# Performance work log

Measured on AMD Instinct MI355X. Metric: run time of the kernel, lower is better.

## Reference

```python
import jax, jax.numpy as jnp
import numpy as np
import math

B_, S_, D_ = 8, 2048, 512
N_ = 16
EXPAND = 1.5
INNER = math.ceil(D_ * EXPAND)  # 768
K_ = 3
DELTA_MIN = 1e-4
DELTA_MAX = 3.0


def _hippo(n):
    A = np.zeros((n, n), np.float32)
    for i in range(n):
        ci = math.sqrt(2 * i + 1)
        for m in range(i + 1):
            cm = math.sqrt(2 * m + 1)
            if i == m:
                A[i, m] = -(2 * i + 1)
            else:
                A[i, m] = (-1.0 if (i - m) % 2 == 0 else 1.0) * ci * cm
    idx = np.arange(n, dtype=np.float32)
    Bv = np.sqrt(2.0 * idx + 1.0)
    Cv = Bv.copy()
    Cv[1::2] *= -1.0
    return A, Bv, Cv


def setup_inputs() -> dict:
    key = jax.random.key(0)
    k0, k1, k2, k3 = jax.random.split(key, 4)
    A0, Bv, Cv = _hippo(N_)
    scale = 1.0 / math.sqrt(INNER)
    return {
        "x": jax.random.normal(k0, (B_, S_, D_), jnp.float32),
        "ln_g": jnp.ones((D_,), jnp.float32),
        "ln_b": jnp.zeros((D_,), jnp.float32),
        "W_in": jax.random.normal(k1, (3 * INNER, D_), jnp.float32) / math.sqrt(D_),
        "conv_w": jax.random.normal(k2, (INNER, 1, K_), jnp.float32) / math.sqrt(K_),
        "A": jnp.asarray(A0),
        "Bmat": jnp.asarray(np.repeat(Bv[:, None], INNER, axis=1) * scale),  # (N, inner)
        "Cmat": jnp.asarray(np.repeat(Cv[None, :], INNER, axis=0) * scale),  # (inner, N)
        "W_out": jax.random.normal(k3, (D_, INNER), jnp.float32) / math.sqrt(INNER),
    }


def reference(x, ln_g, ln_b, W_in, conv_w, A, Bmat, Cmat, W_out):
    B, S, D = x.shape
    N = A.shape[0]
    # LayerNorm
    mu = jnp.mean(x, -1, keepdims=True)
    var = jnp.var(x, -1, keepdims=True)
    h = (x - mu) / jnp.sqrt(var + 1e-5) * ln_g + ln_b
    # Input projection -> data / gate / delta_raw
    proj = h @ W_in.T  # (B,S,3*inner)
    inner = proj.shape[-1] // 3
    data, gate, delta_raw = jnp.split(proj, 3, axis=-1)
    # Depthwise conv with padding K-1 then truncation to S == causal left pad K-1
    K = conv_w.shape[-1]
    dc = jax.lax.conv_general_dilated(
        data.transpose(0, 2, 1), conv_w, window_strides=(1,),
        padding=[(K - 1, 0)], dimension_numbers=("NCH", "OIH", "NCH"),
        feature_group_count=inner,
    ).transpose(0, 2, 1)  # (B,S,inner)
    u = jax.nn.silu(dc)
    # Data-dependent step size
    delta = jnp.mean(jax.nn.softplus(delta_raw), -1, keepdims=True) + DELTA_MIN
    delta = jnp.minimum(delta, DELTA_MAX)  # (B,S,1)
    # ZOH discretisation: A_disc = expm(delta*A); B_disc = A^{-1}(A_disc - I) B
    scaled_A = delta[..., None] * A  # (B,S,N,N)
    A_disc = jax.vmap(jax.scipy.linalg.expm)(scaled_A.reshape(-1, N, N)).reshape(B, S, N, N)
    rhs = A_disc - jnp.eye(N, dtype=x.dtype)
    integral = jnp.linalg.solve(jnp.broadcast_to(A, rhs.shape), rhs)  # (B,S,N,N)
    B_disc = integral @ Bmat  # (B,S,N,inner)

    def step(state, inputs):  # state: (B,N)
        Ad, Bd, ut = inputs  # (B,N,N), (B,N,inner), (B,inner)
        state = jnp.einsum("bnm,bm->bn", Ad, state) + jnp.einsum("bnd,bd->bn", Bd, ut)
        y = jnp.einsum("dn,bn->bd", Cmat, state)  # (B,inner)
        return state, y

    s0 = jnp.zeros((B, N), x.dtype)
    _, ys = jax.lax.scan(
        step, s0,
        (A_disc.transpose(1, 0, 2, 3), B_disc.transpose(1, 0, 2, 3), u.transpose(1, 0, 2)),
    )
    selective = ys.transpose(1, 0, 2)  # (B,S,inner)
    out = (jax.nn.sigmoid(gate) * selective) @ W_out.T
    return x + out
```

## Files before the change

### kernel.cpp

```cpp
#include <hip/hip_runtime.h>
#include <hip/hip_bf16.h>
#include <math.h>

#define BB 8
#define SS 2048
#define DD 512
#define II 768
#define MT (BB*SS)
#define NS 16
#define CH 32
#define NCB (SS/CH)
#define NCHK (MT/CH)
#define NT 1024

typedef __hip_bfloat16 bf16;
typedef __attribute__((ext_vector_type(8))) short bf16x8;
typedef __attribute__((ext_vector_type(4))) float f32x4;

__device__ __forceinline__ float fsigm(float x){
  return __builtin_amdgcn_rcpf(1.f + __expf(-x));
}
__device__ __forceinline__ float fsoftp(float x){
  return (x > 15.f) ? x : __logf(1.f + __expf(x));
}
__device__ __forceinline__ unsigned short f2bf_bits(float f){
  __hip_bfloat16 h = __float2bfloat16(f);
  return __builtin_bit_cast(unsigned short, h);
}
__device__ __forceinline__ float bfbits2f(short s){
  union { float f; unsigned u; } v;
  v.u = ((unsigned)(unsigned short)s) << 16;
  return v.f;
}
__device__ __forceinline__ void gload16(const bf16* src, void* dst){
  __builtin_amdgcn_global_load_lds((const __attribute__((address_space(1))) void*)src,
                                   (__attribute__((address_space(3))) void*)dst, 16, 0, 0);
}
__device__ __forceinline__ void gload16f(const float* src, void* dst){
  __builtin_amdgcn_global_load_lds((const __attribute__((address_space(1))) void*)src,
                                   (__attribute__((address_space(3))) void*)dst, 16, 0, 0);
}
template<int KDIM>
__device__ __forceinline__ bf16x8 lds_a_frag(const bf16* As, int row, int kseg){
  return *(const bf16x8*)((const char*)As + (size_t)row*(KDIM*2)
                          + (size_t)((kseg ^ (row & 7)) << 4));
}

__global__ __launch_bounds__(256) void cast_kernel(
    const float* __restrict__ in, bf16* __restrict__ out, int n4)
{
  int i = blockIdx.x*256 + threadIdx.x;
  if (i >= n4) return;
  float4 v = *(const float4*)&in[(size_t)i*4];
  ushort4 o = make_ushort4(f2bf_bits(v.x), f2bf_bits(v.y), f2bf_bits(v.z), f2bf_bits(v.w));
  *(ushort4*)&out[(size_t)i*4] = o;
}

__global__ __launch_bounds__(256) void bmsplit_kernel(
    const float* __restrict__ Bm, bf16* __restrict__ hi, bf16* __restrict__ lo)
{
  int i = blockIdx.x*256 + threadIdx.x;
  if (i >= NS*II) return;
  float f = Bm[i];
  unsigned short hb = f2bf_bits(f);
  hi[i] = __builtin_bit_cast(bf16, hb);
  lo[i] = __float2bfloat16(f - bfbits2f((short)hb));
}

__global__ __launch_bounds__(256) void apow_kernel(
    const float* __restrict__ A, float* __restrict__ Apow)
{
  __shared__ double Am[256], T0[256], T1[256];
  __shared__ double colsum[16];
  int tid = threadIdx.x, r = tid>>4, c = tid&15;
  double a = (double)A[tid];
  Am[tid] = a; T0[tid] = a;
  Apow[tid] = A[tid];
  __syncthreads();
  double *Tc = T0, *Tn = T1;
  for (int k=2;k<=13;k++){
    double s = 0.0;
    #pragma unroll
    for (int j=0;j<16;j++) s += Tc[r*16+j]*Am[j*16+c];
    Tn[tid] = s;
    Apow[(k-1)*256 + tid] = (float)s;
    __syncthreads();
    double* tmp = Tc; Tc = Tn; Tn = tmp;
  }
  if (tid < 16){
    double s = 0.0;
    #pragma unroll
    for (int j=0;j<16;j++) s += fabs(Am[j*16+tid]);
    colsum[tid] = s;
  }
  __syncthreads();
  if (tid == 0){
    double mx = 0.0;
    #pragma unroll
    for (int j=0;j<16;j++) mx = fmax(mx, colsum[j]);
    Apow[13*256] = (float)mx;
  }
}

__global__ __launch_bounds__(64) void etab_kernel(
    const float* __restrict__ Apow, float* __restrict__ Etab,
    float* __restrict__ Gtab, float* __restrict__ dEtab)
{
  int i = blockIdx.x;
  int l = threadIdx.x;
  int r = l&15, gq = l>>4, c0 = gq*4;
  __shared__ alignas(16) float bufE[256];
  __shared__ alignas(16) float bufG[256];
  float delta = (3.0f*i)/(float)(NT-1);
  float anorm = Apow[13*256];
  float mx = delta*anorm;
  int s = 0;
  if (mx > 2.f){
    s = (int)ceilf(log2f(mx)) - 1;
    if (s < 0) s = 0;
    if (s > 12) s = 12;
  }
  float dsc = ldexpf(delta, -s);
  const float invk[14]  = {0.f, 1.f, 0.5f, 1.f/3.f, 0.25f, 0.2f, 1.f/6.f, 1.f/7.f,
                           0.125f, 1.f/9.f, 0.1f, 1.f/11.f, 1.f/12.f, 1.f/13.f};
  float4 e = make_float4(0.f,0.f,0.f,0.f), g = e;
  if (r==c0  ){ e.x = 1.f; g.x = dsc; }
  if (r==c0+1){ e.y = 1.f; g.y = dsc; }
  if (r==c0+2){ e.z = 1.f; g.z = dsc; }
  if (r==c0+3){ e.w = 1.f; g.w = dsc; }
  float ck = 1.f;
  #pragma unroll
  for (int k=1;k<=13;k++){
    ck *= dsc * invk[k];
    float gk = ck * dsc / (float)(k+1);
    float4 ap = *(const float4*)&Apow[(k-1)*256 + r*16 + c0];
    e.x = fmaf(ck, ap.x, e.x); e.y = fmaf(ck, ap.y, e.y);
    e.z = fmaf(ck, ap.z, e.z); e.w = fmaf(ck, ap.w, e.w);
    g.x = fmaf(gk, ap.x, g.x); g.y = fmaf(gk, ap.y, g.y);
    g.z = fmaf(gk, ap.z, g.z); g.w = fmaf(gk, ap.w, g.w);
  }
  for (int it=0; it<s; ++it){
    *(float4*)&bufE[r*16+c0] = e;
    *(float4*)&bufG[r*16+c0] = g;
    __syncthreads();
    float erow[16];
    #pragma unroll
    for (int q4=0;q4<4;q4++){
      float4 tv = *(const float4*)&bufE[r*16+q4*4];
      erow[q4*4+0]=tv.x; erow[q4*4+1]=tv.y; erow[q4*4+2]=tv.z; erow[q4*4+3]=tv.w;
    }
    float4 en = make_float4(0.f,0.f,0.f,0.f);
    float4 gn = g;
    #pragma unroll
    for (int kk=0;kk<16;kk++){
      float4 ev = *(const float4*)&bufE[kk*16+c0];
      float4 gv = *(const float4*)&bufG[kk*16+c0];
      float ek = erow[kk];
      en.x=fmaf(ek,ev.x,en.x); en.y=fmaf(ek,ev.y,en.y);
      en.z=fmaf(ek,ev.z,en.z); en.w=fmaf(ek,ev.w,en.w);
      gn.x=fmaf(ek,gv.x,gn.x); gn.y=fmaf(ek,gv.y,gn.y);
      gn.z=fmaf(ek,gv.z,gn.z); gn.w=fmaf(ek,gv.w,gn.w);
    }
    e = en; g = gn;
    __syncthreads();
  }
  size_t o = (size_t)i*256 + r*16 + c0;
  *(float4*)&Etab[o] = e;
  *(float4*)&Gtab[o] = g;
  *(float4*)&bufE[r*16+c0] = e;
  __syncthreads();
  float4 de = make_float4(0.f,0.f,0.f,0.f);
  #pragma unroll
  for (int q4=0;q4<4;q4++){
    float4 ar = *(const float4*)&Apow[r*16 + q4*4];
    float4 e0 = *(const float4*)&bufE[(q4*4+0)*16 + c0];
    float4 e1 = *(const float4*)&bufE[(q4*4+1)*16 + c0];
    float4 e2 = *(const float4*)&bufE[(q4*4+2)*16 + c0];
    float4 e3 = *(const float4*)&bufE[(q4*4+3)*16 + c0];
    de.x = fmaf(ar.x,e0.x,fmaf(ar.y,e1.x,fmaf(ar.z,e2.x,fmaf(ar.w,e3.x,de.x))));
    de.y = fmaf(ar.x,e0.y,fmaf(ar.y,e1.y,fmaf(ar.z,e2.y,fmaf(ar.w,e3.y,de.y))));
    de.z = fmaf(ar.x,e0.z,fmaf(ar.y,e1.z,fmaf(ar.z,e2.z,fmaf(ar.w,e3.z,de.z))));
    de.w = fmaf(ar.x,e0.w,fmaf(ar.y,e1.w,fmaf(ar.z,e2.w,fmaf(ar.w,e3.w,de.w))));
  }
  *(float4*)&dEtab[o] = de;
}

__global__ __launch_bounds__(256) void ln_kernel(
    const float* __restrict__ x, const float* __restrict__ g,
    const float* __restrict__ b, bf16* __restrict__ h)
{
  int w = threadIdx.x >> 6, l = threadIdx.x & 63;
  int m = blockIdx.x*4 + w;
  const float* xr = x + (size_t)m*DD;
  float4 v0 = *(const float4*)&xr[l*4];
  float4 v1 = *(const float4*)&xr[256 + l*4];
  float s  = v0.x+v0.y+v0.z+v0.w + v1.x+v1.y+v1.z+v1.w;
  float sq = v0.x*v0.x+v0.y*v0.y+v0.z*v0.z+v0.w*v0.w
           + v1.x*v1.x+v1.y*v1.y+v1.z*v1.z+v1.w*v1.w;
  #pragma unroll
  for (int o=1;o<64;o<<=1){ s += __shfl_xor(s,o); sq += __shfl_xor(sq,o); }
  float mu  = s*(1.f/DD);
  float var = sq*(1.f/DD) - mu*mu;
  float rs  = rsqrtf(var + 1e-5f);
  float4 g0 = *(const float4*)&g[l*4];
  float4 b0 = *(const float4*)&b[l*4];
  float4 g1 = *(const float4*)&g[256 + l*4];
  float4 b1 = *(const float4*)&b[256 + l*4];
  ushort4 o0, o1;
  o0.x = f2bf_bits((v0.x-mu)*rs*g0.x + b0.x);
  o0.y = f2bf_bits((v0.y-mu)*rs*g0.y + b0.y);
  o0.z = f2bf_bits((v0.z-mu)*rs*g0.z + b0.z);
  o0.w = f2bf_bits((v0.w-mu)*rs*g0.w + b0.w);
  o1.x = f2bf_bits((v1.x-mu)*rs*g1.x + b1.x);
  o1.y = f2bf_bits((v1.y-mu)*rs*g1.y + b1.y);
  o1.z = f2bf_bits((v1.z-mu)*rs*g1.z + b1.z);
  o1.w = f2bf_bits((v1.w-mu)*rs*g1.w + b1.w);
  *(ushort4*)&h[(size_t)m*DD + l*4]       = o0;
  *(ushort4*)&h[(size_t)m*DD + 256 + l*4] = o1;
}


__global__ __launch_bounds__(256, 3) void gemm1_mfma(
    const bf16* __restrict__ Ah, const bf16* __restrict__ Bw,
    bf16* __restrict__ databf, bf16* __restrict__ gatebf, float* __restrict__ dacc)
{
  __shared__ alignas(16) bf16 As[128*64];
  __shared__ alignas(16) bf16 Bs[128*64];
  const int tid = threadIdx.x, l = tid & 63, w = tid >> 6;
  const int lrow = l & 15, lgrp = l >> 4;
  const int orig = blockIdx.x;
  const int swz = (orig & 7) * (2304/8) + (orig >> 3);
  const int bm = (swz / 18) * 128;
  const int bn = swz % 18;
  const int wrow = (w >> 1) * 64, wcol = (w & 1) * 64;

  f32x4 acc[4][4];
  #pragma unroll
  for (int i=0;i<4;i++){
    #pragma unroll
    for (int f=0;f<4;f++){ f32x4 z={0.f,0.f,0.f,0.f}; acc[i][f]=z; }
  }

  for (int t=0; t<8; ++t){
    #pragma unroll
    for (int it=0; it<4; ++it){
      int d = tid + it*256;
      int r = d >> 3, s = d & 7;
      gload16(Ah + (size_t)(bm + r)*DD + t*64 + ((s ^ (r&7))<<3),
              (char*)As + (size_t)(d - l)*16);
    }
    #pragma unroll
    for (int it=0; it<4; ++it){
      int d = tid + it*256;
      int r = d >> 3, s = d & 7;
      gload16(Bw + (size_t)(bn*128 + r)*DD + t*64 + ((s ^ (r&7))<<3),
              (char*)Bs + (size_t)(d - l)*16);
    }
    __syncthreads();
    #pragma unroll
    for (int kk=0; kk<2; ++kk){
      bf16x8 afr[4], bfr[4];
      #pragma unroll
      for (int i=0;i<4;i++) afr[i] = lds_a_frag<64>(As, wrow + i*16 + lrow, kk*4 + lgrp);
      #pragma unroll
      for (int f=0;f<4;f++) bfr[f] = lds_a_frag<64>(Bs, wcol + f*16 + lrow, kk*4 + lgrp);
      #pragma unroll
      for (int i=0;i<4;i++){
        #pragma unroll
        for (int f=0;f<4;f++)
          acc[i][f] = __builtin_amdgcn_mfma_f32_16x16x32_bf16(afr[i], bfr[f], acc[i][f], 0,0,0);
      }
    }
    __syncthreads();
  }

  const int rowb = bm + wrow + lgrp*4;
  const int cglob = bn*128 + wcol + lrow;
  if (bn < 6){
    #pragma unroll
    for (int i=0;i<4;i++){
      #pragma unroll
      for (int f=0;f<4;f++){
        int col = cglob + f*16;
        #pragma unroll
        for (int j=0;j<4;j++)
          databf[(size_t)(rowb + i*16 + j)*II + col] = __float2bfloat16(acc[i][f][j]);
      }
    }
  } else if (bn < 12){
    #pragma unroll
    for (int i=0;i<4;i++){
      #pragma unroll
      for (int f=0;f<4;f++){
        int col = cglob - 768 + f*16;
        #pragma unroll
        for (int j=0;j<4;j++)
          gatebf[(size_t)(rowb + i*16 + j)*II + col] = __float2bfloat16(fsigm(acc[i][f][j]));
      }
    }
  } else {
    #pragma unroll
    for (int i=0;i<4;i++){
      #pragma unroll
      for (int j=0;j<4;j++){
        float v = fsoftp(acc[i][0][j]) + fsoftp(acc[i][1][j])
                + fsoftp(acc[i][2][j]) + fsoftp(acc[i][3][j]);
        v += __shfl_xor(v,1); v += __shfl_xor(v,2);
        v += __shfl_xor(v,4); v += __shfl_xor(v,8);
        if (lrow == 0) atomicAdd(&dacc[rowb + i*16 + j], v);
      }
    }
  }
}

__global__ __launch_bounds__(256, 3) void gemm2_mfma(
    const bf16* __restrict__ Asel, const bf16* __restrict__ Bw,
    const float* __restrict__ x, float* __restrict__ out)
{
  __shared__ alignas(16) bf16 As[128*64];
  __shared__ alignas(16) bf16 Bs[128*64];
  const int tid = threadIdx.x, l = tid & 63, w = tid >> 6;
  const int lrow = l & 15, lgrp = l >> 4;
  const int orig = blockIdx.x;
  const int swz = (orig & 7) * (512/8) + (orig >> 3);
  const int bm = (swz >> 2) * 128;
  const int bn = swz & 3;
  const int wrow = (w >> 1) * 64, wcol = (w & 1) * 64;

  f32x4 acc[4][4];
  #pragma unroll
  for (int i=0;i<4;i++){
    #pragma unroll
    for (int f=0;f<4;f++){ f32x4 z={0.f,0.f,0.f,0.f}; acc[i][f]=z; }
  }

  for (int t=0; t<12; ++t){
    #pragma unroll
    for (int it=0; it<4; ++it){
      int d = tid + it*256;
      int r = d >> 3, s = d & 7;
      gload16(Asel + (size_t)(bm + r)*II + t*64 + ((s ^ (r&7))<<3),
              (char*)As + (size_t)(d - l)*16);
    }
    #pragma unroll
    for (int it=0; it<4; ++it){
      int d = tid + it*256;
      int r = d >> 3, s = d & 7;
      gload16(Bw + (size_t)(bn*128 + r)*II + t*64 + ((s ^ (r&7))<<3),
              (char*)Bs + (size_t)(d - l)*16);
    }
    __syncthreads();
    #pragma unroll
    for (int kk=0; kk<2; ++kk){
      bf16x8 afr[4], bfr[4];
      #pragma unroll
      for (int i=0;i<4;i++) afr[i] = lds_a_frag<64>(As, wrow + i*16 + lrow, kk*4 + lgrp);
      #pragma unroll
      for (int f=0;f<4;f++) bfr[f] = lds_a_frag<64>(Bs, wcol + f*16 + lrow, kk*4 + lgrp);
      #pragma unroll
      for (int i=0;i<4;i++){
        #pragma unroll
        for (int f=0;f<4;f++)
          acc[i][f] = __builtin_amdgcn_mfma_f32_16x16x32_bf16(afr[i], bfr[f], acc[i][f], 0,0,0);
      }
    }
    __syncthreads();
  }

  const int rowb = bm + wrow + lgrp*4;
  #pragma unroll
  for (int i=0;i<4;i++){
    #pragma unroll
    for (int f=0;f<4;f++){
      int col = bn*128 + wcol + f*16 + lrow;
      #pragma unroll
      for (int j=0;j<4;j++){
        size_t e = (size_t)(rowb + i*16 + j)*DD + col;
        out[e] = acc[i][f][j] + x[e];
      }
    }
  }
}

__global__ __launch_bounds__(256) void convw_mfma(
    const bf16* __restrict__ data, const float* __restrict__ cw,
    const bf16* __restrict__ Bmhi, const bf16* __restrict__ Bmlo,
    float* __restrict__ w_all)
{
  __shared__ alignas(16) bf16  Ds[1728*8];
  __shared__ alignas(16) float cwl[II*3];
  __shared__ alignas(16) float red[4][256];
  const int tid = threadIdx.x, l = tid & 63, wv = tid >> 6;
  const int lrow = l & 15, lgrp = l >> 4;
  const int p0 = blockIdx.x * 16;
  const int p  = p0 + lrow;
  const int t  = p & (SS-1);
  const int bstart = p0 & ~(SS-1);
  const float mask1 = (t>=1) ? 1.f : 0.f;
  const float mask0 = (t>=2) ? 1.f : 0.f;

  #pragma unroll
  for (int it=0; it<7; ++it){
    int d = tid + it*256;
    if (d < 1728){
      int r = d % 18, s2 = d / 18;
      int prow = p0 - 2 + r; if (prow < bstart) prow = bstart;
      gload16(data + (size_t)prow*II + s2*8, (char*)Ds + (size_t)(d - l)*16);
    }
  }
  #pragma unroll
  for (int it=0; it<3; ++it){
    int d = tid + it*256;
    if (d < 576)
      gload16f(cw + d*4, (char*)cwl + (size_t)(d - l)*16);
  }
  __syncthreads();

  const int sB = wv*24 + lgrp;
  const char* DsB = (const char*)Ds + ((size_t)sB*18 + lrow)*16;
  const bf16* bh  = Bmhi + (size_t)lrow*II + sB*8;
  const bf16* bl  = Bmlo + (size_t)lrow*II + sB*8;
  const float* cwp = cwl + sB*24;

  f32x4 acc = {0.f,0.f,0.f,0.f};
  #pragma unroll
  for (int u=0; u<6; ++u){
    bf16x8 v0 = *(const bf16x8*)(DsB + (size_t)u*72*16);
    bf16x8 v1 = *(const bf16x8*)(DsB + (size_t)u*72*16 + 16);
    bf16x8 v2 = *(const bf16x8*)(DsB + (size_t)u*72*16 + 32);
    bf16x8 ah = *(const bf16x8*)(bh + u*32);
    bf16x8 al = *(const bf16x8*)(bl + u*32);
    float cv[24];
    #pragma unroll
    for (int q=0;q<6;q++){
      float4 cq = *(const float4*)(cwp + u*96 + q*4);
      cv[q*4+0]=cq.x; cv[q*4+1]=cq.y; cv[q*4+2]=cq.z; cv[q*4+3]=cq.w;
    }
    bf16x8 Bh, Bl;
    #pragma unroll
    for (int j=0;j<8;j++){
      float d2 = bfbits2f(v2[j]);
      float d1 = bfbits2f(v1[j]) * mask1;
      float d0 = bfbits2f(v0[j]) * mask0;
      float a = fmaf(d0, cv[3*j], fmaf(d1, cv[3*j+1], d2*cv[3*j+2]));
      float u2 = a * fsigm(a);
      unsigned short hb = f2bf_bits(u2);
      Bh[j] = (short)hb;
      Bl[j] = (short)f2bf_bits(u2 - bfbits2f((short)hb));
    }
    acc = __builtin_amdgcn_mfma_f32_16x16x32_bf16(ah, Bh, acc, 0,0,0);
    acc = __builtin_amdgcn_mfma_f32_16x16x32_bf16(ah, Bl, acc, 0,0,0);
    acc = __builtin_amdgcn_mfma_f32_16x16x32_bf16(al, Bh, acc, 0,0,0);
  }
  *(f32x4*)&red[wv][l*4] = acc;
  __syncthreads();
  if (wv == 0){
    f32x4 s0 = *(const f32x4*)&red[0][l*4];
    f32x4 s1 = *(const f32x4*)&red[1][l*4];
    f32x4 s2 = *(const f32x4*)&red[2][l*4];
    f32x4 s3 = *(const f32x4*)&red[3][l*4];
    f32x4 s = s0 + s1 + s2 + s3;
    *(f32x4*)&w_all[(size_t)p*NS + lgrp*4] = s;
  }
}

__global__ __launch_bounds__(256) void scan1_kernel(
    const float* __restrict__ Etab, const float* __restrict__ Gtab,
    const float* __restrict__ dEtab, const float* __restrict__ dacc,
    const float* __restrict__ w_all,
    float* __restrict__ Ad, float* __restrict__ c_all,
    float* __restrict__ P, float* __restrict__ q)
{
  int cc = blockIdx.x;
  int bb = cc / NCB, ci = cc % NCB;
  size_t base = (size_t)bb*SS + (size_t)ci*CH;
  int tid = threadIdx.x;
  int i = tid>>4, j = tid&15;
  __shared__ float Et[CH][256];
  __shared__ float cb[CH][16];
  __shared__ float Pb[2][256];
  __shared__ float qb[2][16];
  Pb[0][tid] = (i==j)?1.f:0.f;
  if (tid<16) qb[0][tid]=0.f;
  const float hh = 3.f/(float)(NT-1);
  for (int t=0;t<CH;t++){
    size_t m = base + t;
    float delta = fminf(dacc[m]*(1.f/II) + 1e-4f, 3.0f);
    float tf = delta * (float)(NT-1) * (1.f/3.f);
    int i0 = (int)tf;
    if (i0 > NT-2) i0 = NT-2;
    float fr = tf - (float)i0;
    float fr2 = fr*fr, fr3 = fr2*fr;
    float h00 = 2.f*fr3 - 3.f*fr2 + 1.f;
    float h10 = fr3 - 2.f*fr2 + fr;
    float h01 = -2.f*fr3 + 3.f*fr2;
    float h11 = fr3 - fr2;
    size_t o0 = (size_t)i0*256 + tid;
    float E0 = Etab[o0], E1 = Etab[o0+256];
    float D0 = dEtab[o0], D1 = dEtab[o0+256];
    float G0 = Gtab[o0], G1 = Gtab[o0+256];
    float e = h00*E0 + h01*E1 + hh*(h10*D0 + h11*D1);
    float g = h00*G0 + h01*G1 + hh*(h10*E0 + h11*E1);
    Ad[m*256 + tid] = e;
    Et[t][j*16 + i] = e;
    float cv = g * w_all[m*NS + j];
    cv += __shfl_xor(cv,1); cv += __shfl_xor(cv,2);
    cv += __shfl_xor(cv,4); cv += __shfl_xor(cv,8);
    if (j==0){ c_all[m*NS + i] = cv; cb[t][i] = cv; }
  }
  __syncthreads();
  int cur = 0;
  for (int t=0;t<CH;t++){
    float acc2 = 0.f;
    #pragma unroll
    for (int k=0;k<16;k++) acc2 = fmaf(Et[t][k*16+i], Pb[cur][k*16+j], acc2);
    float qa = 0.f;
    if (j==0){
      #pragma unroll
      for (int k=0;k<16;k++) qa = fmaf(Et[t][k*16+i], qb[cur][k], qa);
      qa += cb[t][i];
    }
    Pb[cur^1][tid] = acc2;
    if (j==0) qb[cur^1][i] = qa;
    __syncthreads();
    cur ^= 1;
  }
  P[(size_t)cc*256 + tid] = Pb[cur][tid];
  if (tid<16) q[(size_t)cc*NS + tid] = qb[cur][tid];
}

__global__ __launch_bounds__(64) void scan2_kernel(
    const float* __restrict__ P, const float* __restrict__ q,
    float* __restrict__ entry)
{
  int b = blockIdx.x;
  int l = threadIdx.x;
  __shared__ alignas(16) float Pl[2][256];
  __shared__ float el[2][16];
  if (l < 16) el[0][l] = 0.f;
  gload16f(P + (size_t)(b*NCB)*256 + l*4, (char*)Pl[0]);
  float qv = q[(size_t)(b*NCB)*NS + (l & 15)];
  int cur = 0;
  for (int ci=0; ci<NCB; ci++){
    __syncthreads();
    int cc = b*NCB + ci;
    if (ci+1 < NCB)
      gload16f(P + (size_t)(cc+1)*256 + l*4, (char*)Pl[cur^1]);
    float qn = (ci+1 < NCB) ? q[(size_t)(cc+1)*NS + (l&15)] : 0.f;
    if (l < 16){
      entry[(size_t)cc*NS + l] = el[cur][l];
      float a = qv;
      #pragma unroll
      for (int k=0;k<16;k++) a = fmaf(Pl[cur][l*16+k], el[cur][k], a);
      el[cur^1][l] = a;
    }
    qv = qn;
    cur ^= 1;
  }
}

__global__ __launch_bounds__(256) void scan3sel_kernel(
    const float* __restrict__ Ad, const float* __restrict__ c_all,
    const float* __restrict__ entry, const float* __restrict__ Cm,
    const bf16* __restrict__ gate, bf16* __restrict__ selg)
{
  __shared__ alignas(16) float Ads[CH*256];
  __shared__ alignas(16) float cl[CH*16];
  int cc = blockIdx.x;
  int bb = cc / NCB, ci = cc % NCB;
  size_t base = (size_t)bb*SS + (size_t)ci*CH;
  int tid = threadIdx.x, l = tid & 63, w = tid >> 6;
  int r = l & 15;
  const float* Adc = Ad + base*256;
  #pragma unroll
  for (int it=0; it<8; ++it){
    int d = tid + it*256;
    int tt = d >> 6, rr = (d >> 2) & 15, k4 = d & 3;
    gload16f(Adc + tt*256 + rr*16 + ((k4 ^ ((rr>>1)&3))<<2),
             (char*)Ads + (size_t)(d - l)*16);
  }
  {
    int d = tid;
    if (d < 128)
      gload16f(c_all + base*NS + d*4, (char*)cl + (size_t)(d - l)*16);
  }
  float g[16];
  #pragma unroll
  for (int k=0;k<16;k++) g[k] = entry[(size_t)cc*NS + k];
  __syncthreads();

  const int frm = (r>>1)&3;
  for (int t=0;t<CH;t++){
    size_t m = base + t;
    float s = cl[t*16 + r];
    #pragma unroll
    for (int q4=0;q4<4;q4++){
      float4 ev = *(const float4*)&Ads[(t*64 + r*4 + (q4 ^ frm))*4];
      s = fmaf(ev.x, g[q4*4+0], s);
      s = fmaf(ev.y, g[q4*4+1], s);
      s = fmaf(ev.z, g[q4*4+2], s);
      s = fmaf(ev.w, g[q4*4+3], s);
    }
    #pragma unroll
    for (int k=0;k<16;k++) g[k] = __shfl(s, k);
    #pragma unroll
    for (int p=0;p<3;p++){
      int jcol = w*192 + p*64 + l;
      float y = 0.f;
      #pragma unroll
      for (int q4=0;q4<4;q4++){
        float4 cv = *(const float4*)&Cm[jcol*16 + q4*4];
        y = fmaf(cv.x, g[q4*4+0], y);
        y = fmaf(cv.y, g[q4*4+1], y);
        y = fmaf(cv.z, g[q4*4+2], y);
        y = fmaf(cv.w, g[q4*4+3], y);
      }
      size_t e = m*II + jcol;
      float gv = __bfloat162float(gate[e]);
      selg[e] = __float2bfloat16(gv*y);
    }
  }
}

extern "C" void kernel_launch(void* const* d_in, const int* in_sizes, int n_in,
                              void* d_out, int out_size, void* d_ws, size_t ws_size,
                              hipStream_t stream) {
  (void)in_sizes; (void)n_in; (void)out_size; (void)ws_size;
  const float* x      = (const float*)d_in[0];
  const float* ln_g   = (const float*)d_in[1];
  const float* ln_b   = (const float*)d_in[2];
  const float* W_in   = (const float*)d_in[3];
  const float* conv_w = (const float*)d_in[4];
  const float* A      = (const float*)d_in[5];
  const float* Bm     = (const float*)d_in[6];
  const float* Cm     = (const float*)d_in[7];
  const float* Wout   = (const float*)d_in[8];
  float* out = (float*)d_out;

  char* ws = (char*)d_ws;
  size_t off = 0;
  #define WSALLOC(ty, name, count) \
    ty* name = (ty*)(ws + off); off += (((size_t)(count))*sizeof(ty) + 255) & ~(size_t)255;
  WSALLOC(bf16,  hbf,    (size_t)MT*DD)
  WSALLOC(bf16,  databf, (size_t)MT*II)
  WSALLOC(bf16,  gatebf, (size_t)MT*II)
  WSALLOC(float, dacc,   MT)
  WSALLOC(float, w_all,  (size_t)MT*NS)
  WSALLOC(float, Ad,     (size_t)MT*256)
  WSALLOC(float, c_all,  (size_t)MT*NS)
  WSALLOC(float, Pbuf,   (size_t)NCHK*256)
  WSALLOC(float, qbuf,   (size_t)NCHK*NS)
  WSALLOC(float, entry,  (size_t)NCHK*NS)
  WSALLOC(bf16,  Winbf,  (size_t)3*II*DD)
  WSALLOC(bf16,  Woutbf, (size_t)DD*II)
  WSALLOC(bf16,  Bmhi,   (size_t)NS*II)
  WSALLOC(bf16,  Bmlo,   (size_t)NS*II)
  WSALLOC(float, Apow,   13*256 + 16)
  WSALLOC(float, Etab,   (size_t)NT*256)
  WSALLOC(float, Gtab,   (size_t)NT*256)
  WSALLOC(float, dEtab,  (size_t)NT*256)
  #undef WSALLOC

  hipMemsetAsync(dacc, 0, (size_t)MT*sizeof(float), stream);
  cast_kernel  <<<(3*II*DD/4 + 255)/256, 256, 0, stream>>>(W_in,  Winbf,  3*II*DD/4);
  cast_kernel  <<<(DD*II/4   + 255)/256, 256, 0, stream>>>(Wout,  Woutbf, DD*II/4);
  bmsplit_kernel<<<(NS*II + 255)/256, 256, 0, stream>>>(Bm, Bmhi, Bmlo);
  apow_kernel  <<<1, 256, 0, stream>>>(A, Apow);
  etab_kernel  <<<NT, 64, 0, stream>>>(Apow, Etab, Gtab, dEtab);
  ln_kernel    <<<MT/4, 256, 0, stream>>>(x, ln_g, ln_b, hbf);
  gemm1_mfma   <<<dim3(2304), 256, 0, stream>>>(hbf, Winbf, databf, gatebf, dacc);
  convw_mfma   <<<MT/16, 256, 0, stream>>>(databf, conv_w, Bmhi, Bmlo, w_all);
  scan1_kernel <<<NCHK, 256, 0, stream>>>(Etab, Gtab, dEtab, dacc, w_all, Ad, c_all, Pbuf, qbuf);
  scan2_kernel <<<BB, 64, 0, stream>>>(Pbuf, qbuf, entry);
  scan3sel_kernel<<<NCHK, 256, 0, stream>>>(Ad, c_all, entry, Cm, gatebf, databf);
  gemm2_mfma   <<<dim3(512), 256, 0, stream>>>(databf, Woutbf, x, out);
}
```

Before: 206.9 us.

## Split scan3sel into single-wave state recurrence and parallel output phase

The chunk scan kernel now runs the 16-state recurrence in one wave only and stores each step's state into shared memory. After a barrier, all 256 threads compute the C-projection and gating for the 32 timesteps, each thread owning three contiguous columns whose C rows are held in registers. Before, every one of the four waves redundantly recomputed the recurrence and reloaded C from global memory at every step. The trade is a serial phase where three waves sit idle, plus strided per-thread gate and output accesses (three consecutive bf16 per thread) that may coalesce worse than the earlier lane-contiguous pattern.

```diff
diff --git a/kernel.cpp b/kernel.cpp
--- a/kernel.cpp
+++ b/kernel.cpp
@@ -566,10 +566,11 @@
 {
   __shared__ alignas(16) float Ads[CH*256];
   __shared__ alignas(16) float cl[CH*16];
+  __shared__ alignas(16) float Gs[CH][16];
   int cc = blockIdx.x;
   int bb = cc / NCB, ci = cc % NCB;
   size_t base = (size_t)bb*SS + (size_t)ci*CH;
-  int tid = threadIdx.x, l = tid & 63, w = tid >> 6;
+  int tid = threadIdx.x, l = tid & 63;
   int r = l & 15;
   const float* Adc = Ad + base*256;
   #pragma unroll
@@ -579,45 +580,61 @@
     gload16f(Adc + tt*256 + rr*16 + ((k4 ^ ((rr>>1)&3))<<2),
              (char*)Ads + (size_t)(d - l)*16);
   }
-  {
-    int d = tid;
-    if (d < 128)
-      gload16f(c_all + base*NS + d*4, (char*)cl + (size_t)(d - l)*16);
-  }
-  float g[16];
-  #pragma unroll
-  for (int k=0;k<16;k++) g[k] = entry[(size_t)cc*NS + k];
-  __syncthreads();
-
-  const int frm = (r>>1)&3;
+  if (tid < 128)
+    gload16f(c_all + base*NS + tid*4, (char*)cl + (size_t)(tid - l)*16);
+
+  float cmr[3][16];
+  #pragma unroll
+  for (int p=0;p<3;p++){
+    int jcol = tid*3 + p;
+    #pragma unroll
+    for (int q4=0;q4<4;q4++){
+      float4 cv = *(const float4*)&Cm[jcol*16 + q4*4];
+      cmr[p][q4*4+0]=cv.x; cmr[p][q4*4+1]=cv.y;
+      cmr[p][q4*4+2]=cv.z; cmr[p][q4*4+3]=cv.w;
+    }
+  }
+  __syncthreads();
+
+  if (tid < 64){
+    float g[16];
+    #pragma unroll
+    for (int k=0;k<16;k++) g[k] = entry[(size_t)cc*NS + k];
+    const int frm = (r>>1)&3;
+    for (int t=0;t<CH;t++){
+      float s = cl[t*16 + r];
+      #pragma unroll
+      for (int q4=0;q4<4;q4++){
+        float4 ev = *(const float4*)&Ads[(t*64 + r*4 + (q4 ^ frm))*4];
+        s = fmaf(ev.x, g[q4*4+0], s);
+        s = fmaf(ev.y, g[q4*4+1], s);
+        s = fmaf(ev.z, g[q4*4+2], s);
+        s = fmaf(ev.w, g[q4*4+3], s);
+      }
+      #pragma unroll
+      for (int k=0;k<16;k++) g[k] = __shfl(s, k);
+      if (l < 16) Gs[t][l] = s;
+    }
+  }
+  __syncthreads();
+
+  const int col0 = tid*3;
+  const bf16* gp = gate + base*II + col0;
+  bf16* sp = selg + base*II + col0;
   for (int t=0;t<CH;t++){
-    size_t m = base + t;
-    float s = cl[t*16 + r];
+    float gk[16];
     #pragma unroll
     for (int q4=0;q4<4;q4++){
-      float4 ev = *(const float4*)&Ads[(t*64 + r*4 + (q4 ^ frm))*4];
-      s = fmaf(ev.x, g[q4*4+0], s);
-      s = fmaf(ev.y, g[q4*4+1], s);
-      s = fmaf(ev.z, g[q4*4+2], s);
-      s = fmaf(ev.w, g[q4*4+3], s);
-    }
-    #pragma unroll
-    for (int k=0;k<16;k++) g[k] = __shfl(s, k);
+      float4 gv4 = *(const float4*)&Gs[t][q4*4];
+      gk[q4*4+0]=gv4.x; gk[q4*4+1]=gv4.y; gk[q4*4+2]=gv4.z; gk[q4*4+3]=gv4.w;
+    }
     #pragma unroll
     for (int p=0;p<3;p++){
-      int jcol = w*192 + p*64 + l;
       float y = 0.f;
       #pragma unroll
-      for (int q4=0;q4<4;q4++){
-        float4 cv = *(const float4*)&Cm[jcol*16 + q4*4];
-        y = fmaf(cv.x, g[q4*4+0], y);
-        y = fmaf(cv.y, g[q4*4+1], y);
-        y = fmaf(cv.z, g[q4*4+2], y);
-        y = fmaf(cv.w, g[q4*4+3], y);
-      }
-      size_t e = m*II + jcol;
-      float gv = __bfloat162float(gate[e]);
-      selg[e] = __float2bfloat16(gv*y);
+      for (int k=0;k<16;k++) y = fmaf(cmr[p][k], gk[k], y);
+      float gv = __bfloat162float(gp[(size_t)t*II + p]);
+      sp[(size_t)t*II + p] = __float2bfloat16(gv*y);
     }
   }
 }
```

Measured after the change: 211.8 us. 2.4% more time.

## Recompute discretised A in scan3 instead of storing it to global memory

Applied to the files above, without the earlier changes.

Drops the per-timestep 16x16 A_disc buffer that scan1 wrote to global memory and scan3 read back, and recomputes it in scan3 by interpolating the cached tables into a swizzled shared-memory layout. Also keeps each thread's Cmat rows in registers rather than reloading them every timestep. This removes a large global write and read, but duplicates the interpolation work and increases register pressure in scan3.

```diff
diff --git a/kernel.cpp b/kernel.cpp
--- a/kernel.cpp
+++ b/kernel.cpp
@@ -468,8 +468,7 @@
     const float* __restrict__ Etab, const float* __restrict__ Gtab,
     const float* __restrict__ dEtab, const float* __restrict__ dacc,
     const float* __restrict__ w_all,
-    float* __restrict__ Ad, float* __restrict__ c_all,
-    float* __restrict__ P, float* __restrict__ q)
+    float* __restrict__ c_all, float* __restrict__ P, float* __restrict__ q)
 {
   int cc = blockIdx.x;
   int bb = cc / NCB, ci = cc % NCB;
@@ -501,7 +500,6 @@
     float G0 = Gtab[o0], G1 = Gtab[o0+256];
     float e = h00*E0 + h01*E1 + hh*(h10*D0 + h11*D1);
     float g = h00*G0 + h01*G1 + hh*(h10*E0 + h11*E1);
-    Ad[m*256 + tid] = e;
     Et[t][j*16 + i] = e;
     float cv = g * w_all[m*NS + j];
     cv += __shfl_xor(cv,1); cv += __shfl_xor(cv,2);
@@ -560,7 +558,8 @@
 }
 
 __global__ __launch_bounds__(256) void scan3sel_kernel(
-    const float* __restrict__ Ad, const float* __restrict__ c_all,
+    const float* __restrict__ Etab, const float* __restrict__ dEtab,
+    const float* __restrict__ dacc, const float* __restrict__ c_all,
     const float* __restrict__ entry, const float* __restrict__ Cm,
     const bf16* __restrict__ gate, bf16* __restrict__ selg)
 {
@@ -571,18 +570,41 @@
   size_t base = (size_t)bb*SS + (size_t)ci*CH;
   int tid = threadIdx.x, l = tid & 63, w = tid >> 6;
   int r = l & 15;
-  const float* Adc = Ad + base*256;
-  #pragma unroll
-  for (int it=0; it<8; ++it){
-    int d = tid + it*256;
-    int tt = d >> 6, rr = (d >> 2) & 15, k4 = d & 3;
-    gload16f(Adc + tt*256 + rr*16 + ((k4 ^ ((rr>>1)&3))<<2),
-             (char*)Ads + (size_t)(d - l)*16);
-  }
-  {
-    int d = tid;
-    if (d < 128)
-      gload16f(c_all + base*NS + d*4, (char*)cl + (size_t)(d - l)*16);
+  int i = tid >> 4, j = tid & 15;
+  if (tid < 128)
+    gload16f(c_all + base*NS + tid*4, (char*)cl + (size_t)(tid - l)*16);
+
+  float cmr[3][16];
+  #pragma unroll
+  for (int p=0;p<3;p++){
+    int jcol = w*192 + p*64 + l;
+    #pragma unroll
+    for (int q4=0;q4<4;q4++){
+      float4 cv = *(const float4*)&Cm[jcol*16 + q4*4];
+      cmr[p][q4*4+0]=cv.x; cmr[p][q4*4+1]=cv.y;
+      cmr[p][q4*4+2]=cv.z; cmr[p][q4*4+3]=cv.w;
+    }
+  }
+
+  const float hh = 3.f/(float)(NT-1);
+  const int wslot = (j>>2) ^ ((i>>1)&3);
+  const int woff  = i*16 + wslot*4 + (j&3);
+  for (int t=0;t<CH;t++){
+    size_t m = base + t;
+    float delta = fminf(dacc[m]*(1.f/II) + 1e-4f, 3.0f);
+    float tf = delta * (float)(NT-1) * (1.f/3.f);
+    int i0 = (int)tf;
+    if (i0 > NT-2) i0 = NT-2;
+    float fr = tf - (float)i0;
+    float fr2 = fr*fr, fr3 = fr2*fr;
+    float h00 = 2.f*fr3 - 3.f*fr2 + 1.f;
+    float h10 = fr3 - 2.f*fr2 + fr;
+    float h01 = -2.f*fr3 + 3.f*fr2;
+    float h11 = fr3 - fr2;
+    size_t o0 = (size_t)i0*256 + tid;
+    float E0 = Etab[o0], E1 = Etab[o0+256];
+    float D0 = dEtab[o0], D1 = dEtab[o0+256];
+    Ads[t*256 + woff] = h00*E0 + h01*E1 + hh*(h10*D0 + h11*D1);
   }
   float g[16];
   #pragma unroll
@@ -608,13 +630,7 @@
       int jcol = w*192 + p*64 + l;
       float y = 0.f;
       #pragma unroll
-      for (int q4=0;q4<4;q4++){
-        float4 cv = *(const float4*)&Cm[jcol*16 + q4*4];
-        y = fmaf(cv.x, g[q4*4+0], y);
-        y = fmaf(cv.y, g[q4*4+1], y);
-        y = fmaf(cv.z, g[q4*4+2], y);
-        y = fmaf(cv.w, g[q4*4+3], y);
-      }
+      for (int k=0;k<16;k++) y = fmaf(cmr[p][k], g[k], y);
       size_t e = m*II + jcol;
       float gv = __bfloat162float(gate[e]);
       selg[e] = __float2bfloat16(gv*y);
@@ -646,7 +662,6 @@
   WSALLOC(bf16,  gatebf, (size_t)MT*II)
   WSALLOC(float, dacc,   MT)
   WSALLOC(float, w_all,  (size_t)MT*NS)
-  WSALLOC(float, Ad,     (size_t)MT*256)
   WSALLOC(float, c_all,  (size_t)MT*NS)
   WSALLOC(float, Pbuf,   (size_t)NCHK*256)
   WSALLOC(float, qbuf,   (size_t)NCHK*NS)
@@ -670,8 +685,8 @@
   ln_kernel    <<<MT/4, 256, 0, stream>>>(x, ln_g, ln_b, hbf);
   gemm1_mfma   <<<dim3(2304), 256, 0, stream>>>(hbf, Winbf, databf, gatebf, dacc);
   convw_mfma   <<<MT/16, 256, 0, stream>>>(databf, conv_w, Bmhi, Bmlo, w_all);
-  scan1_kernel <<<NCHK, 256, 0, stream>>>(Etab, Gtab, dEtab, dacc, w_all, Ad, c_all, Pbuf, qbuf);
+  scan1_kernel <<<NCHK, 256, 0, stream>>>(Etab, Gtab, dEtab, dacc, w_all, c_all, Pbuf, qbuf);
   scan2_kernel <<<BB, 64, 0, stream>>>(Pbuf, qbuf, entry);
-  scan3sel_kernel<<<NCHK, 256, 0, stream>>>(Ad, c_all, entry, Cm, gatebf, databf);
+  scan3sel_kernel<<<NCHK, 256, 0, stream>>>(Etab, dEtab, dacc, c_all, entry, Cm, gatebf, databf);
   gemm2_mfma   <<<dim3(512), 256, 0, stream>>>(databf, Woutbf, x, out);
 }
```

New measurement: 207.9 us. About the same (+0.5%).
